# Kernel tuning notes

Hardware: AMD Instinct MI355X
Metric: run time of the kernel (lower is better)

## Reference

```python
import jax, jax.numpy as jnp
import numpy as np

SIZES = [4096, 12288, 20480, 20480, 8192]  # atoms of degree 0..4 (atoms sorted by degree)
N_ATOMS = sum(SIZES)
BATCH = 1024
N_TASKS, N_CLASSES = 12, 2
BN_EPS = 1e-3  # keras BatchNormalization default epsilon


def setup_inputs() -> dict:
    key = jax.random.key(0)
    ks = jax.random.split(key, 20)
    inp = {}
    inp["atom_features"] = jax.random.normal(ks[0], (N_ATOMS, 75), jnp.float32)
    starts = np.concatenate([[0], np.cumsum(SIZES)[:-1]])
    inp["degree_slice"] = jnp.asarray(np.stack([starts, np.array(SIZES)], 1), jnp.int32)
    inp["membership"] = jax.random.randint(ks[1], (N_ATOMS,), 0, BATCH, jnp.int32)
    inp["n_samples"] = BATCH
    for d in range(1, 5):
        inp[f"deg_adj_{d}"] = jax.random.randint(ks[1 + d], (SIZES[d], d), 0, N_ATOMS, jnp.int32)

    def w(k, shape, s=0.05):
        return s * jax.random.normal(k, shape, jnp.float32)

    # GraphConv weights: order [relW_deg1, selfW_deg1, ..., relW_deg4, selfW_deg4, selfW_deg0]
    inp["gc1_W"] = w(ks[6], (9, 75, 256)); inp["gc1_b"] = w(ks[7], (9, 256))
    inp["gc2_W"] = w(ks[8], (9, 256, 256)); inp["gc2_b"] = w(ks[9], (9, 256))

    def bn_params(k, c):  # rows: gamma, beta, moving_mean, moving_var
        g = 1.0 + 0.1 * jax.random.normal(k, (c,), jnp.float32)
        b = 0.1 * jax.random.normal(jax.random.fold_in(k, 1), (c,), jnp.float32)
        return jnp.stack([g, b, jnp.zeros((c,), jnp.float32), jnp.ones((c,), jnp.float32)])

    inp["bn1"] = bn_params(ks[10], 256)
    inp["bn2"] = bn_params(ks[11], 256)
    inp["bn3"] = bn_params(ks[12], 512)
    inp["dense_W"] = w(ks[13], (256, 512)); inp["dense_b"] = w(ks[14], (512,))
    inp["head_W"] = w(ks[15], (2 * 512, N_TASKS * N_CLASSES)); inp["head_b"] = w(ks[16], (N_TASKS * N_CLASSES,))
    return inp


def _graph_conv(x, adjs, W, b):
    # degree-0 atoms: self transform only (last weight matrix)
    pieces = [x[: SIZES[0]] @ W[8] + b[8]]
    off = SIZES[0]
    for d in range(1, 5):
        nd = SIZES[d]
        self_atoms = x[off: off + nd]
        rel = jnp.take(x, adjs[d - 1], axis=0).sum(axis=1)  # [nd, F] neighbor sum
        out = rel @ W[2 * (d - 1)] + b[2 * (d - 1)] + self_atoms @ W[2 * d - 1] + b[2 * d - 1]
        pieces.append(out)
        off += nd
    return jax.nn.relu(jnp.concatenate(pieces, axis=0))


def _graph_pool(x, adjs):
    pieces = [x[: SIZES[0]]]  # degree-0: passthrough
    off = SIZES[0]
    for d in range(1, 5):
        nd = SIZES[d]
        self_atoms = x[off: off + nd]
        neigh = jnp.take(x, adjs[d - 1], axis=0)  # [nd, d, F]
        pieces.append(jnp.maximum(self_atoms, neigh.max(axis=1)))
        off += nd
    return jnp.concatenate(pieces, axis=0)


def _bn(x, p):  # inference batchnorm with moving stats
    g, b, m, v = p
    return g * (x - m) * jax.lax.rsqrt(v + BN_EPS) + b


def reference(atom_features, degree_slice, membership, n_samples,
              deg_adj_1, deg_adj_2, deg_adj_3, deg_adj_4,
              gc1_W, gc1_b, gc2_W, gc2_b, bn1, bn2, bn3,
              dense_W, dense_b, head_W, head_b):
    adjs = (deg_adj_1, deg_adj_2, deg_adj_3, deg_adj_4)
    x = atom_features
    for W, b, bn in ((gc1_W, gc1_b, bn1), (gc2_W, gc2_b, bn2)):
        x = _bn(_graph_conv(x, adjs, W, b), bn)
        x = _graph_pool(x, adjs)
    h = _bn(jax.nn.relu(x @ dense_W + dense_b), bn3)  # [N_ATOMS, 512]
    # GraphGather: per-molecule sum and max, tanh activation
    seg_sum = jax.ops.segment_sum(h, membership, num_segments=BATCH)
    seg_max = jax.ops.segment_max(h, membership, num_segments=BATCH)
    fp = jnp.tanh(jnp.concatenate([seg_sum, seg_max], axis=1))  # neural fingerprint [BATCH, 1024]
    logits = (fp @ head_W + head_b).reshape(BATCH, N_TASKS, N_CLASSES)[: int(n_samples)]  # trim
    return jax.nn.softmax(logits, axis=-1), logits, fp
```

## Files before the change

kernel.cpp:

```cpp
#include <hip/hip_runtime.h>
#include <hip/hip_bf16.h>
#include <math.h>

#define NA 65536
#define MAXSEG 160

typedef _Float16 half8 __attribute__((ext_vector_type(8)));
typedef _Float16 h4    __attribute__((ext_vector_type(4)));
typedef float float4v  __attribute__((ext_vector_type(4)));

typedef __attribute__((address_space(3))) unsigned int lds_uint;
typedef __attribute__((address_space(1))) const unsigned int g_uint;

__device__ __forceinline__ void async16(const void* g, void* l) {
    __builtin_amdgcn_global_load_lds((g_uint*)g, (lds_uint*)l, 16, 0, 0);
}


__device__ __forceinline__ int unperm128(int p) {
    return (p & ~127) + (((p & 127) & 7) << 4) + ((p & 127) >> 3);
}

__device__ __forceinline__ unsigned mapf(float x) {
    unsigned b = __float_as_uint(x);
    return (b & 0x80000000u) ? ~b : (b | 0x80000000u);
}
#define MAPF_NEGINF 0x007FFFFFu

__device__ __forceinline__ void atom_seg(int atom, int& d, int& loc,
                                         const int* a1, const int* a2,
                                         const int* a3, const int* a4,
                                         const int*& adj) {
    if (atom < 4096)       { d = 0; loc = 0; adj = nullptr; }
    else if (atom < 16384) { d = 1; adj = a1; loc = atom - 4096; }
    else if (atom < 36864) { d = 2; adj = a2; loc = atom - 16384; }
    else if (atom < 57344) { d = 3; adj = a3; loc = atom - 36864; }
    else                   { d = 4; adj = a4; loc = atom - 57344; }
}

__global__ __launch_bounds__(256) void prep_kernel(
    const float* __restrict__ af,
    const float* __restrict__ gc1W, const float* __restrict__ gc1b,
    const float* __restrict__ gc2W, const float* __restrict__ gc2b,
    const float* __restrict__ dW, const float* __restrict__ hW,
    _Float16* __restrict__ af16, _Float16* __restrict__ Wc1, float* __restrict__ bias1,
    _Float16* __restrict__ Wc2, float* __restrict__ bias2,
    _Float16* __restrict__ dWt, float* __restrict__ hWt, int* __restrict__ count,
    float* __restrict__ fpsum, unsigned* __restrict__ fpmaxu) {
    int b = blockIdx.x, t = threadIdx.x;
    if (b < 5120) {
        int idx = b * 256 + t;
        int atom = idx / 20, k4 = idx - atom * 20;
        int c0 = k4 * 4;
        h4 o;
        #pragma unroll
        for (int j = 0; j < 4; j++) {
            int c = c0 + j;
            o[j] = (_Float16)((c < 75) ? af[(size_t)atom * 75 + c] : 0.f);
        }
        *(h4*)(af16 + (size_t)atom * 80 + c0) = o;
    } else if (b < 5920) {
        int idx = (b - 5120) * 256 + t;
        if (idx < 204800) {
            int k = idx % 160, n = (idx / 160) & 255, seg = idx / (160 * 256);
            float v = 0.f;
            if (k < 80) {
                if (k < 75) { int w = (seg == 0) ? 8 : (2 * seg - 1); v = gc1W[(w * 75 + k) * 256 + n]; }
            } else {
                int kk = k - 80;
                if (kk < 75 && seg > 0) { int w = 2 * (seg - 1); v = gc1W[(w * 75 + kk) * 256 + n]; }
            }
            Wc1[(size_t)(seg * 256 + n) * 160 + k] = (_Float16)v;
        }
        if (idx < 1280) {
            int n = idx & 255, seg = idx >> 8;
            bias1[idx] = (seg == 0) ? gc1b[8 * 256 + n]
                                    : gc1b[(2 * seg - 1) * 256 + n] + gc1b[2 * (seg - 1) * 256 + n];
        }
    } else if (b < 8480) {
        int idx = (b - 5920) * 256 + t;
        int k = idx & 511, n = (idx >> 9) & 255, seg = idx >> 17;
        float v = 0.f;
        if (k < 256) {
            int w = (seg == 0) ? 8 : (2 * seg - 1);
            v = gc2W[(w * 256 + unperm128(k)) * 256 + n];
        } else if (seg > 0) {
            int w = 2 * (seg - 1);
            v = gc2W[(w * 256 + unperm128(k - 256)) * 256 + n];
        }
        Wc2[(size_t)(seg * 256 + n) * 512 + k] = (_Float16)v;
        if (idx < 1280) {
            int nn = idx & 255, sg = idx >> 8;
            bias2[idx] = (sg == 0) ? gc2b[8 * 256 + nn]
                                   : gc2b[(2 * sg - 1) * 256 + nn] + gc2b[2 * (sg - 1) * 256 + nn];
        }
    } else if (b < 8992) {
        int idx = (b - 8480) * 256 + t;
        int n = idx >> 8, k = idx & 255;
        dWt[(size_t)n * 256 + k] = (_Float16)dW[(size_t)unperm128(k) * 512 + n];
    } else if (b < 9088) {
        int idx = (b - 8992) * 256 + t;
        int o = idx / 1024, k = idx & 1023;
        hWt[idx] = hW[k * 24 + o];
    } else if (b < 9092) {
        int i = (b - 9088) * 256 + t;
        if (i < 1024) count[i] = 0;
    } else if (b < 11140) {
        fpsum[(size_t)(b - 9092) * 256 + t] = 0.f;
    } else {
        fpmaxu[(size_t)(b - 11140) * 256 + t] = MAPF_NEGINF;
    }
}

__global__ void bucket_kernel(const int* __restrict__ mem, int* __restrict__ count,
                              int* __restrict__ list) {
    int i = blockIdx.x * 256 + threadIdx.x;
    int seg = mem[i];
    int pos = atomicAdd(&count[seg], 1);
    if (pos < MAXSEG) list[seg * MAXSEG + pos] = i;
}

__global__ __launch_bounds__(1024) void scan_kernel(const int* __restrict__ count,
                                                    int* __restrict__ offs) {
    __shared__ int tmp[1024];
    int t = threadIdx.x;
    int v = count[t]; if (v > MAXSEG) v = MAXSEG;
    tmp[t] = v;
    __syncthreads();
    for (int off = 1; off < 1024; off <<= 1) {
        int x = (t >= off) ? tmp[t - off] : 0;
        __syncthreads();
        tmp[t] += x;
        __syncthreads();
    }
    offs[t] = tmp[t] - v;
}

__global__ __launch_bounds__(256) void build_sorted_kernel(
    const int* __restrict__ count, const int* __restrict__ offs,
    const int* __restrict__ list, int* __restrict__ sorted) {
    int seg = blockIdx.x;
    int n = count[seg]; if (n > MAXSEG) n = MAXSEG;
    int base = offs[seg];
    for (int i = threadIdx.x; i < n; i += 256)
        sorted[base + i] = list[seg * MAXSEG + i] | (seg << 16);
}

__global__ __launch_bounds__(256) void gather1n_kernel(
    const _Float16* __restrict__ af16,
    const int* __restrict__ a1, const int* __restrict__ a2,
    const int* __restrict__ a3, const int* __restrict__ a4,
    _Float16* __restrict__ Xn1) {
    int idx = blockIdx.x * 256 + threadIdx.x;
    int atom = idx / 20, k4 = idx - atom * 20;
    int c0 = k4 * 4;
    int d, loc; const int* adj;
    atom_seg(atom, d, loc, a1, a2, a3, a4, adj);
    float s0 = 0.f, s1 = 0.f, s2 = 0.f, s3 = 0.f;
    for (int j = 0; j < d; j++) {
        int nb = adj[(size_t)loc * d + j];
        h4 v = *(const h4*)(af16 + (size_t)nb * 80 + c0);
        s0 += (float)v[0]; s1 += (float)v[1]; s2 += (float)v[2]; s3 += (float)v[3];
    }
    h4 o; o[0] = (_Float16)s0; o[1] = (_Float16)s1; o[2] = (_Float16)s2; o[3] = (_Float16)s3;
    *(h4*)(Xn1 + (size_t)atom * 80 + c0) = o;
}

template<int K, int N, int BK, int SB>
__global__ __launch_bounds__(256) void gemm_kernel(
    const _Float16* __restrict__ X, const _Float16* __restrict__ Xn,
    const _Float16* __restrict__ Wt,
    const float* __restrict__ bias, const float* __restrict__ bnp,
    int wstride, int bstride, _Float16* __restrict__ out) {
    constexpr int NC8 = BK / 8;
    constexpr int MASK = NC8 - 1;
    __shared__ __align__(16) _Float16 As[128 * BK];
    __shared__ __align__(16) _Float16 Bs[128 * BK];
    constexpr int nb = N / 128;
    int G = gridDim.x;
    int bid = (blockIdx.x & 7) * (G >> 3) + (blockIdx.x >> 3);
    int m0 = (bid / nb) * 128, n0 = (bid % nb) * 128;
    int t = m0 >> 7;
    int seg = (t < 32) ? 0 : (t < 128) ? 1 : (t < 288) ? 2 : (t < 448) ? 3 : 4;
    const _Float16* Wb = Wt + (size_t)seg * wstride;
    const float* bia = bias + seg * bstride;
    int tid = threadIdx.x, lane = tid & 63, wave = tid >> 6;
    int wm = (wave >> 1) * 64, wn = (wave & 1) * 64;
    int lrow = lane & 15, lq = lane >> 4;
    float4v acc[4][4] = {};
    for (int kc = 0; kc < K / BK; kc++) {
        #pragma unroll
        for (int q = 0; q < NC8 / 2; q++) {
            int slot = q * 256 + wave * 64 + lane;
            int row = slot / NC8;
            int cs = slot & MASK;
            int c8 = cs ^ (row & MASK);
            const _Float16* gA;
            if (SB == 0) {
                gA = X + (size_t)(m0 + row) * K + kc * BK + c8 * 8;
            } else {
                int kcol = kc * BK + c8 * 8;
                gA = (kcol < SB) ? X  + (size_t)(m0 + row) * SB + kcol
                                 : Xn + (size_t)(m0 + row) * SB + (kcol - SB);
            }
            async16(gA, As + (size_t)(q * 256 + wave * 64) * 8);
            const _Float16* gB = Wb + (size_t)(n0 + row) * K + kc * BK + c8 * 8;
            async16(gB, Bs + (size_t)(q * 256 + wave * 64) * 8);
        }
        __syncthreads();
        #pragma unroll
        for (int kl = 0; kl < BK / 32; kl++) {
            half8 af[4], bf[4];
            #pragma unroll
            for (int i = 0; i < 4; i++) {
                int ra = wm + i * 16 + lrow;
                int ca = (kl * 4 + lq) ^ (ra & MASK);
                af[i] = *(const half8*)(As + ra * BK + ca * 8);
                int rb = wn + i * 16 + lrow;
                int cb = (kl * 4 + lq) ^ (rb & MASK);
                bf[i] = *(const half8*)(Bs + rb * BK + cb * 8);
            }
            #pragma unroll
            for (int mi = 0; mi < 4; mi++)
                #pragma unroll
                for (int ni = 0; ni < 4; ni++)
                    acc[mi][ni] = __builtin_amdgcn_mfma_f32_16x16x32_f16(af[mi], bf[ni], acc[mi][ni], 0, 0, 0);
        }
        __syncthreads();
    }
    float bv[4], sc[4], mn[4], be[4];
    #pragma unroll
    for (int ni = 0; ni < 4; ni++) {
        int c = n0 + wn + ni * 16 + lrow;
        bv[ni] = bia[c];
        float g = bnp[c], vr = bnp[3 * N + c];
        mn[ni] = bnp[2 * N + c]; be[ni] = bnp[N + c];
        sc[ni] = g * rsqrtf(vr + 1e-3f);
    }
    int p0 = n0 + lrow * 8 + (wave & 1) * 4;
    #pragma unroll
    for (int mi = 0; mi < 4; mi++) {
        #pragma unroll
        for (int r = 0; r < 4; r++) {
            h4 pack;
            #pragma unroll
            for (int ni = 0; ni < 4; ni++) {
                float v = acc[mi][ni][r] + bv[ni];
                v = fmaxf(v, 0.f);
                v = sc[ni] * (v - mn[ni]) + be[ni];
                pack[ni] = (_Float16)v;
            }
            int row = m0 + wm + mi * 16 + lq * 4 + r;
            *(h4*)(out + (size_t)row * N + p0) = pack;
        }
    }
}

__global__ __launch_bounds__(256, 2) void gemm2_kernel(
    const _Float16* __restrict__ p, const _Float16* __restrict__ Wt,
    const float* __restrict__ bias, const float* __restrict__ bnp,
    const int* __restrict__ a1, const int* __restrict__ a2,
    const int* __restrict__ a3, const int* __restrict__ a4,
    _Float16* __restrict__ out) {
    __shared__ __align__(16) _Float16 As[128 * 64];
    __shared__ __align__(16) _Float16 Bs[256 * 64];
    int G = gridDim.x;
    int bid = (blockIdx.x & 7) * (G >> 3) + (blockIdx.x >> 3);
    int m0 = bid * 128;
    int t8 = m0 >> 7;
    int seg = (t8 < 32) ? 0 : (t8 < 128) ? 1 : (t8 < 288) ? 2 : (t8 < 448) ? 3 : 4;
    int segstart = (seg == 0) ? 0 : (seg == 1) ? 4096 : (seg == 2) ? 16384 : (seg == 3) ? 36864 : 57344;
    const int* adj = (seg == 1) ? a1 : (seg == 2) ? a2 : (seg == 3) ? a3 : (seg == 4) ? a4 : nullptr;
    int d = seg;
    int loc0 = m0 - segstart;
    const _Float16* Wb = Wt + (size_t)seg * 256 * 512;
    const float* bia = bias + seg * 256;
    int tid = threadIdx.x, lane = tid & 63, wave = tid >> 6;
    int wm = (wave >> 1) * 64, wn = (wave & 1) * 128;
    int lrow = lane & 15, lq = lane >> 4;
    float4v acc[4][8] = {};
    for (int kc = 0; kc < 8; kc++) {
        if (kc < 4) {
            #pragma unroll
            for (int q = 0; q < 4; q++) {
                int slot = q * 256 + wave * 64 + lane;
                int row = slot >> 3, cs = slot & 7, c8 = cs ^ (row & 7);
                async16(p + (size_t)(m0 + row) * 256 + kc * 64 + c8 * 8,
                        As + (size_t)(q * 256 + wave * 64) * 8);
            }
        } else {
            #pragma unroll
            for (int q = 0; q < 4; q++) {
                int slot = q * 256 + wave * 64 + lane;
                int row = slot >> 3, cs = slot & 7, c8 = cs ^ (row & 7);
                int col = (kc - 4) * 64 + c8 * 8;
                float s[8] = {};
                for (int j = 0; j < d; j++) {
                    int nb = adj[(size_t)(loc0 + row) * d + j];
                    half8 v = *(const half8*)(p + (size_t)nb * 256 + col);
                    #pragma unroll
                    for (int e = 0; e < 8; e++) s[e] += (float)v[e];
                }
                half8 o;
                #pragma unroll
                for (int e = 0; e < 8; e++) o[e] = (_Float16)s[e];
                *(half8*)(As + row * 64 + cs * 8) = o;
            }
        }
        #pragma unroll
        for (int q = 0; q < 8; q++) {
            int slot = q * 256 + wave * 64 + lane;
            int row = slot >> 3, cs = slot & 7, c8 = cs ^ (row & 7);
            async16(Wb + (size_t)row * 512 + kc * 64 + c8 * 8,
                    Bs + (size_t)(q * 256 + wave * 64) * 8);
        }
        __syncthreads();
        #pragma unroll
        for (int kl = 0; kl < 2; kl++) {
            half8 af[4], bf[8];
            #pragma unroll
            for (int i = 0; i < 4; i++) {
                int ra = wm + i * 16 + lrow;
                int ca = (kl * 4 + lq) ^ (ra & 7);
                af[i] = *(const half8*)(As + ra * 64 + ca * 8);
            }
            #pragma unroll
            for (int j = 0; j < 8; j++) {
                int rb = wn + j * 16 + lrow;
                int cb = (kl * 4 + lq) ^ (rb & 7);
                bf[j] = *(const half8*)(Bs + rb * 64 + cb * 8);
            }
            #pragma unroll
            for (int mi = 0; mi < 4; mi++)
                #pragma unroll
                for (int ni = 0; ni < 8; ni++)
                    acc[mi][ni] = __builtin_amdgcn_mfma_f32_16x16x32_f16(af[mi], bf[ni], acc[mi][ni], 0, 0, 0);
        }
        __syncthreads();
    }
    float bv[8], sc[8], mn[8], be[8];
    #pragma unroll
    for (int ni = 0; ni < 8; ni++) {
        int c = wn + ni * 16 + lrow;
        bv[ni] = bia[c];
        float g = bnp[c], vr = bnp[3 * 256 + c];
        mn[ni] = bnp[2 * 256 + c]; be[ni] = bnp[256 + c];
        sc[ni] = g * rsqrtf(vr + 1e-3f);
    }
    int p0 = wn + lrow * 8;
    #pragma unroll
    for (int mi = 0; mi < 4; mi++) {
        #pragma unroll
        for (int r = 0; r < 4; r++) {
            half8 pack;
            #pragma unroll
            for (int ni = 0; ni < 8; ni++) {
                float v = acc[mi][ni][r] + bv[ni];
                v = fmaxf(v, 0.f);
                v = sc[ni] * (v - mn[ni]) + be[ni];
                pack[ni] = (_Float16)v;
            }
            int row = m0 + wm + mi * 16 + lq * 4 + r;
            *(half8*)(out + (size_t)row * 256 + p0) = pack;
        }
    }
}

__global__ __launch_bounds__(256) void pool_f16_kernel(
    const _Float16* __restrict__ x,
    const int* __restrict__ a1, const int* __restrict__ a2,
    const int* __restrict__ a3, const int* __restrict__ a4,
    _Float16* __restrict__ out) {
    int atom = blockIdx.x * 8 + (threadIdx.x >> 5);
    int l = threadIdx.x & 31;
    int d, loc; const int* adj;
    atom_seg(atom, d, loc, a1, a2, a3, a4, adj);
    half8 m = *(const half8*)(x + (size_t)atom * 256 + l * 8);
    float mv[8];
    #pragma unroll
    for (int e = 0; e < 8; e++) mv[e] = (float)m[e];
    for (int j = 0; j < d; j++) {
        int nb = adj[(size_t)loc * d + j];
        half8 v = *(const half8*)(x + (size_t)nb * 256 + l * 8);
        #pragma unroll
        for (int e = 0; e < 8; e++) mv[e] = fmaxf(mv[e], (float)v[e]);
    }
    half8 o;
    #pragma unroll
    for (int e = 0; e < 8; e++) o[e] = (_Float16)mv[e];
    *(half8*)(out + (size_t)atom * 256 + l * 8) = o;
}

__global__ __launch_bounds__(256) void dense_kernel(
    const _Float16* __restrict__ X, const _Float16* __restrict__ Wt,
    const float* __restrict__ bias, const float* __restrict__ bnp,
    const int* __restrict__ sorted,
    float* __restrict__ fpsum, unsigned* __restrict__ fpmaxu) {
    constexpr int NBINS = 32;
    __shared__ __align__(16) _Float16 As[128 * 64];
    __shared__ __align__(16) _Float16 Bs[128 * 64];
    __shared__ float binsum[NBINS * 128];
    __shared__ unsigned binmax[NBINS * 128];
    __shared__ int spk[128];
    int G = gridDim.x;
    int bid = (blockIdx.x & 7) * (G >> 3) + (blockIdx.x >> 3);
    int m0 = (bid >> 2) * 128, n0 = (bid & 3) * 128;
    int tid = threadIdx.x, lane = tid & 63, wave = tid >> 6;
    if (tid < 128) spk[tid] = sorted[m0 + tid];
    for (int e = tid; e < NBINS * 128; e += 256) { binsum[e] = 0.f; binmax[e] = MAPF_NEGINF; }
    __syncthreads();
    const _Float16* baseA[4]; const _Float16* baseB[4];
    #pragma unroll
    for (int q = 0; q < 4; q++) {
        int slot = q * 256 + wave * 64 + lane;
        int row = slot >> 3, cs = slot & 7, c8 = cs ^ (row & 7);
        baseA[q] = X + (size_t)(spk[row] & 0xFFFF) * 256 + c8 * 8;
        baseB[q] = Wt + (size_t)(n0 + row) * 256 + c8 * 8;
    }
    int wm = (wave >> 1) * 64, wn = (wave & 1) * 64;
    int lrow = lane & 15, lq = lane >> 4;
    float4v acc[4][4] = {};
    for (int kc = 0; kc < 4; kc++) {
        #pragma unroll
        for (int q = 0; q < 4; q++) {
            async16(baseA[q] + kc * 64, As + (size_t)(q * 256 + wave * 64) * 8);
            async16(baseB[q] + kc * 64, Bs + (size_t)(q * 256 + wave * 64) * 8);
        }
        __syncthreads();
        #pragma unroll
        for (int kl = 0; kl < 2; kl++) {
            half8 af[4], bf[4];
            #pragma unroll
            for (int i = 0; i < 4; i++) {
                int ra = wm + i * 16 + lrow;
                int ca = (kl * 4 + lq) ^ (ra & 7);
                af[i] = *(const half8*)(As + ra * 64 + ca * 8);
                int rb = wn + i * 16 + lrow;
                int cb = (kl * 4 + lq) ^ (rb & 7);
                bf[i] = *(const half8*)(Bs + rb * 64 + cb * 8);
            }
            #pragma unroll
            for (int mi = 0; mi < 4; mi++)
                #pragma unroll
                for (int ni = 0; ni < 4; ni++)
                    acc[mi][ni] = __builtin_amdgcn_mfma_f32_16x16x32_f16(af[mi], bf[ni], acc[mi][ni], 0, 0, 0);
        }
        __syncthreads();
    }
    float bv[4], sc[4], mn[4], be[4];
    #pragma unroll
    for (int ni = 0; ni < 4; ni++) {
        int c = n0 + wn + ni * 16 + lrow;
        bv[ni] = bias[c];
        float g = bnp[c], vr = bnp[3 * 512 + c];
        mn[ni] = bnp[2 * 512 + c]; be[ni] = bnp[512 + c];
        sc[ni] = g * rsqrtf(vr + 1e-3f);
    }
    int pcol = lrow * 8 + (wave & 1) * 4;
    int segbase = spk[0] >> 16;
    int curs = -1;
    float ps[4], pm[4];
    #pragma unroll
    for (int mi = 0; mi < 4; mi++) {
        #pragma unroll
        for (int r = 0; r < 4; r++) {
            int row = wm + mi * 16 + lq * 4 + r;
            int srel = (spk[row] >> 16) - segbase;
            if (srel > NBINS - 1) srel = NBINS - 1;
            if (srel != curs) {
                if (curs >= 0) {
                    int bb = curs * 128 + pcol;
                    #pragma unroll
                    for (int ni = 0; ni < 4; ni++) {
                        atomicAdd(&binsum[bb + ni], ps[ni]);
                        atomicMax(&binmax[bb + ni], mapf(pm[ni]));
                    }
                }
                curs = srel;
                #pragma unroll
                for (int ni = 0; ni < 4; ni++) { ps[ni] = 0.f; pm[ni] = -INFINITY; }
            }
            #pragma unroll
            for (int ni = 0; ni < 4; ni++) {
                float v = acc[mi][ni][r] + bv[ni];
                v = fmaxf(v, 0.f);
                v = sc[ni] * (v - mn[ni]) + be[ni];
                ps[ni] += v;
                pm[ni] = fmaxf(pm[ni], v);
            }
        }
    }
    {
        int bb = curs * 128 + pcol;
        #pragma unroll
        for (int ni = 0; ni < 4; ni++) {
            atomicAdd(&binsum[bb + ni], ps[ni]);
            atomicMax(&binmax[bb + ni], mapf(pm[ni]));
        }
    }
    __syncthreads();
    int nseg = (spk[127] >> 16) - segbase + 1;
    if (nseg > NBINS) nseg = NBINS;
    for (int e = tid; e < nseg * 128; e += 256) {
        int s = e >> 7, pc = e & 127;
        float v = binsum[e];
        if (v != 0.f) atomicAdd(&fpsum[(size_t)(segbase + s) * 512 + n0 + pc], v);
        unsigned u = binmax[e];
        if (u != MAPF_NEGINF) atomicMax(&fpmaxu[(size_t)(segbase + s) * 512 + n0 + pc], u);
    }
}

__global__ __launch_bounds__(256) void head_kernel(
    const float* __restrict__ fpsum, const unsigned* __restrict__ fpmaxu,
    const float* __restrict__ hWt, const float* __restrict__ hb,
    float* __restrict__ fp, float* __restrict__ logits, float* __restrict__ probs) {
    __shared__ float fps[1024];
    __shared__ float red[32];
    int s = blockIdx.x;
    for (int i = threadIdx.x; i < 512; i += 256) {
        float sv = tanhf(fpsum[(size_t)s * 512 + i]);
        unsigned u = fpmaxu[(size_t)s * 512 + i];
        unsigned b = (u & 0x80000000u) ? (u & 0x7FFFFFFFu) : ~u;
        float mv = tanhf(__uint_as_float(b));
        int chan = unperm128(i);
        fps[chan] = sv; fps[512 + chan] = mv;
        fp[(size_t)s * 1024 + chan] = sv;
        fp[(size_t)s * 1024 + 512 + chan] = mv;
    }
    __syncthreads();
    int t = threadIdx.x;
    int o = t >> 3, kp = t & 7;
    float acc = 0.f;
    if (o < 24) {
        const float* w = hWt + (size_t)o * 1024 + kp * 128;
        const float* f = fps + kp * 128;
        #pragma unroll 8
        for (int i = 0; i < 128; i++) acc = fmaf(f[i], w[i], acc);
    }
    acc += __shfl_down(acc, 4, 64);
    acc += __shfl_down(acc, 2, 64);
    acc += __shfl_down(acc, 1, 64);
    if (o < 24 && kp == 0) red[o] = acc + hb[o];
    __syncthreads();
    if (t < 24) {
        float a = red[t];
        float an = red[t ^ 1];
        logits[(size_t)s * 24 + t] = a;
        probs[(size_t)s * 24 + t] = 1.f / (1.f + expf(an - a));
    }
}

extern "C" void kernel_launch(void* const* d_in, const int* in_sizes, int n_in,
                              void* d_out, int out_size, void* d_ws, size_t ws_size,
                              hipStream_t stream) {
    const float* af         = (const float*)d_in[0];
    const int*   membership = (const int*)d_in[2];
    const int*   a1 = (const int*)d_in[4];
    const int*   a2 = (const int*)d_in[5];
    const int*   a3 = (const int*)d_in[6];
    const int*   a4 = (const int*)d_in[7];
    const float* gc1W = (const float*)d_in[8];
    const float* gc1b = (const float*)d_in[9];
    const float* gc2W = (const float*)d_in[10];
    const float* gc2b = (const float*)d_in[11];
    const float* bn1  = (const float*)d_in[12];
    const float* bn2  = (const float*)d_in[13];
    const float* bn3  = (const float*)d_in[14];
    const float* dW   = (const float*)d_in[15];
    const float* db   = (const float*)d_in[16];
    const float* hW   = (const float*)d_in[17];
    const float* hb   = (const float*)d_in[18];

    float* out    = (float*)d_out;
    float* probs  = out;
    float* logits = out + 24576;
    float* fp     = out + 49152;

    _Float16* Wc1  = (_Float16*)d_ws;
    _Float16* Wc2  = Wc1 + 204800;
    _Float16* dWt  = Wc2 + 655360;
    float* bias1   = (float*)(dWt + 131072);
    float* bias2   = bias1 + 1280;
    float* hWt     = bias2 + 1280;
    float* fpsum   = hWt + 24576;
    unsigned* fpmaxu = (unsigned*)(fpsum + 524288);
    int* count     = (int*)(fpmaxu + 524288);
    int* offs      = count + 1024;
    int* sorted    = offs + 1024;
    int* list      = sorted + 65536;
    _Float16* bufSm  = (_Float16*)(list + 163840);
    _Float16* bufY   = bufSm + (size_t)NA * 160;
    _Float16* bufP   = bufY + (size_t)NA * 256;
    _Float16* af16 = bufSm;
    _Float16* Xn1  = bufSm + (size_t)NA * 80;

    prep_kernel<<<13188, 256, 0, stream>>>(af, gc1W, gc1b, gc2W, gc2b, dW, hW,
                                           af16, Wc1, bias1, Wc2, bias2, dWt, hWt,
                                           count, fpsum, fpmaxu);
    bucket_kernel<<<256, 256, 0, stream>>>(membership, count, list);
    scan_kernel<<<1, 1024, 0, stream>>>(count, offs);
    build_sorted_kernel<<<1024, 256, 0, stream>>>(count, offs, list, sorted);
    gather1n_kernel<<<5120, 256, 0, stream>>>(af16, a1, a2, a3, a4, Xn1);
    gemm_kernel<160, 256, 32, 80><<<1024, 256, 0, stream>>>(af16, Xn1, Wc1, bias1, bn1,
                                                            256 * 160, 256, bufY);
    pool_f16_kernel<<<8192, 256, 0, stream>>>(bufY, a1, a2, a3, a4, bufP);
    gemm2_kernel<<<512, 256, 0, stream>>>(bufP, Wc2, bias2, bn2, a1, a2, a3, a4, bufY);
    pool_f16_kernel<<<8192, 256, 0, stream>>>(bufY, a1, a2, a3, a4, bufP);
    dense_kernel<<<2048, 256, 0, stream>>>(bufP, dWt, db, bn3, sorted, fpsum, fpmaxu);
    head_kernel<<<1024, 256, 0, stream>>>(fpsum, fpmaxu, hWt, hb, fp, logits, probs);
}
```

Measured before the change: 321.8 us.

## Split layer-2 neighbor gather out of fused GEMM into separate gather kernel

```diff
diff --git a/kernel.cpp b/kernel.cpp
--- a/kernel.cpp
+++ b/kernel.cpp
@@ -164,6 +164,28 @@
     }
     h4 o; o[0] = (_Float16)s0; o[1] = (_Float16)s1; o[2] = (_Float16)s2; o[3] = (_Float16)s3;
     *(h4*)(Xn1 + (size_t)atom * 80 + c0) = o;
+}
+
+__global__ __launch_bounds__(256) void gather2n_kernel(
+    const _Float16* __restrict__ p,
+    const int* __restrict__ a1, const int* __restrict__ a2,
+    const int* __restrict__ a3, const int* __restrict__ a4,
+    _Float16* __restrict__ Xn) {
+    int atom = blockIdx.x * 8 + (threadIdx.x >> 5);
+    int l = threadIdx.x & 31;
+    int d, loc; const int* adj;
+    atom_seg(atom, d, loc, a1, a2, a3, a4, adj);
+    float s[8] = {};
+    for (int j = 0; j < d; j++) {
+        int nb = adj[(size_t)loc * d + j];
+        half8 v = *(const half8*)(p + (size_t)nb * 256 + l * 8);
+        #pragma unroll
+        for (int e = 0; e < 8; e++) s[e] += (float)v[e];
+    }
+    half8 o;
+    #pragma unroll
+    for (int e = 0; e < 8; e++) o[e] = (_Float16)s[e];
+    *(half8*)(Xn + (size_t)atom * 256 + l * 8) = o;
 }
 
 template<int K, int N, int BK, int SB>
@@ -256,116 +278,6 @@
     }
 }
 
-__global__ __launch_bounds__(256, 2) void gemm2_kernel(
-    const _Float16* __restrict__ p, const _Float16* __restrict__ Wt,
-    const float* __restrict__ bias, const float* __restrict__ bnp,
-    const int* __restrict__ a1, const int* __restrict__ a2,
-    const int* __restrict__ a3, const int* __restrict__ a4,
-    _Float16* __restrict__ out) {
-    __shared__ __align__(16) _Float16 As[128 * 64];
-    __shared__ __align__(16) _Float16 Bs[256 * 64];
-    int G = gridDim.x;
-    int bid = (blockIdx.x & 7) * (G >> 3) + (blockIdx.x >> 3);
-    int m0 = bid * 128;
-    int t8 = m0 >> 7;
-    int seg = (t8 < 32) ? 0 : (t8 < 128) ? 1 : (t8 < 288) ? 2 : (t8 < 448) ? 3 : 4;
-    int segstart = (seg == 0) ? 0 : (seg == 1) ? 4096 : (seg == 2) ? 16384 : (seg == 3) ? 36864 : 57344;
-    const int* adj = (seg == 1) ? a1 : (seg == 2) ? a2 : (seg == 3) ? a3 : (seg == 4) ? a4 : nullptr;
-    int d = seg;
-    int loc0 = m0 - segstart;
-    const _Float16* Wb = Wt + (size_t)seg * 256 * 512;
-    const float* bia = bias + seg * 256;
-    int tid = threadIdx.x, lane = tid & 63, wave = tid >> 6;
-    int wm = (wave >> 1) * 64, wn = (wave & 1) * 128;
-    int lrow = lane & 15, lq = lane >> 4;
-    float4v acc[4][8] = {};
-    for (int kc = 0; kc < 8; kc++) {
-        if (kc < 4) {
-            #pragma unroll
-            for (int q = 0; q < 4; q++) {
-                int slot = q * 256 + wave * 64 + lane;
-                int row = slot >> 3, cs = slot & 7, c8 = cs ^ (row & 7);
-                async16(p + (size_t)(m0 + row) * 256 + kc * 64 + c8 * 8,
-                        As + (size_t)(q * 256 + wave * 64) * 8);
-            }
-        } else {
-            #pragma unroll
-            for (int q = 0; q < 4; q++) {
-                int slot = q * 256 + wave * 64 + lane;
-                int row = slot >> 3, cs = slot & 7, c8 = cs ^ (row & 7);
-                int col = (kc - 4) * 64 + c8 * 8;
-                float s[8] = {};
-                for (int j = 0; j < d; j++) {
-                    int nb = adj[(size_t)(loc0 + row) * d + j];
-                    half8 v = *(const half8*)(p + (size_t)nb * 256 + col);
-                    #pragma unroll
-                    for (int e = 0; e < 8; e++) s[e] += (float)v[e];
-                }
-                half8 o;
-                #pragma unroll
-                for (int e = 0; e < 8; e++) o[e] = (_Float16)s[e];
-                *(half8*)(As + row * 64 + cs * 8) = o;
-            }
-        }
-        #pragma unroll
-        for (int q = 0; q < 8; q++) {
-            int slot = q * 256 + wave * 64 + lane;
-            int row = slot >> 3, cs = slot & 7, c8 = cs ^ (row & 7);
-            async16(Wb + (size_t)row * 512 + kc * 64 + c8 * 8,
-                    Bs + (size_t)(q * 256 + wave * 64) * 8);
-        }
-        __syncthreads();
-        #pragma unroll
-        for (int kl = 0; kl < 2; kl++) {
-            half8 af[4], bf[8];
-            #pragma unroll
-            for (int i = 0; i < 4; i++) {
-                int ra = wm + i * 16 + lrow;
-                int ca = (kl * 4 + lq) ^ (ra & 7);
-                af[i] = *(const half8*)(As + ra * 64 + ca * 8);
-            }
-            #pragma unroll
-            for (int j = 0; j < 8; j++) {
-                int rb = wn + j * 16 + lrow;
-                int cb = (kl * 4 + lq) ^ (rb & 7);
-                bf[j] = *(const half8*)(Bs + rb * 64 + cb * 8);
-            }
-            #pragma unroll
-            for (int mi = 0; mi < 4; mi++)
-                #pragma unroll
-                for (int ni = 0; ni < 8; ni++)
-                    acc[mi][ni] = __builtin_amdgcn_mfma_f32_16x16x32_f16(af[mi], bf[ni], acc[mi][ni], 0, 0, 0);
-        }
-        __syncthreads();
-    }
-    float bv[8], sc[8], mn[8], be[8];
-    #pragma unroll
-    for (int ni = 0; ni < 8; ni++) {
-        int c = wn + ni * 16 + lrow;
-        bv[ni] = bia[c];
-        float g = bnp[c], vr = bnp[3 * 256 + c];
-        mn[ni] = bnp[2 * 256 + c]; be[ni] = bnp[256 + c];
-        sc[ni] = g * rsqrtf(vr + 1e-3f);
-    }
-    int p0 = wn + lrow * 8;
-    #pragma unroll
-    for (int mi = 0; mi < 4; mi++) {
-        #pragma unroll
-        for (int r = 0; r < 4; r++) {
-            half8 pack;
-            #pragma unroll
-            for (int ni = 0; ni < 8; ni++) {
-                float v = acc[mi][ni][r] + bv[ni];
-                v = fmaxf(v, 0.f);
-                v = sc[ni] * (v - mn[ni]) + be[ni];
-                pack[ni] = (_Float16)v;
-            }
-            int row = m0 + wm + mi * 16 + lq * 4 + r;
-            *(half8*)(out + (size_t)row * 256 + p0) = pack;
-        }
-    }
-}
-
 __global__ __launch_bounds__(256) void pool_f16_kernel(
     const _Float16* __restrict__ x,
     const int* __restrict__ a1, const int* __restrict__ a2,
@@ -589,7 +501,8 @@
     int* sorted    = offs + 1024;
     int* list      = sorted + 65536;
     _Float16* bufSm  = (_Float16*)(list + 163840);
-    _Float16* bufY   = bufSm + (size_t)NA * 160;
+    _Float16* Xn     = bufSm + (size_t)NA * 160;
+    _Float16* bufY   = Xn + (size_t)NA * 256;
     _Float16* bufP   = bufY + (size_t)NA * 256;
     _Float16* af16 = bufSm;
     _Float16* Xn1  = bufSm + (size_t)NA * 80;
@@ -604,7 +517,9 @@
     gemm_kernel<160, 256, 32, 80><<<1024, 256, 0, stream>>>(af16, Xn1, Wc1, bias1, bn1,
                                                             256 * 160, 256, bufY);
     pool_f16_kernel<<<8192, 256, 0, stream>>>(bufY, a1, a2, a3, a4, bufP);
-    gemm2_kernel<<<512, 256, 0, stream>>>(bufP, Wc2, bias2, bn2, a1, a2, a3, a4, bufY);
+    gather2n_kernel<<<8192, 256, 0, stream>>>(bufP, a1, a2, a3, a4, Xn);
+    gemm_kernel<512, 256, 64, 256><<<1024, 256, 0, stream>>>(bufP, Xn, Wc2, bias2, bn2,
+                                                             256 * 512, 256, bufY);
     pool_f16_kernel<<<8192, 256, 0, stream>>>(bufY, a1, a2, a3, a4, bufP);
     dense_kernel<<<2048, 256, 0, stream>>>(bufP, dWt, db, bn3, sorted, fpsum, fpmaxu);
     head_kernel<<<1024, 256, 0, stream>>>(fpsum, fpmaxu, hWt, hb, fp, logits, probs);
```

Measured after the change: 307.6 us. -4.4%, faster.
